# Optimization experiments

Hardware: AMD Instinct MI355X
Metric: run time of the kernel (lower is better)

Reference implementation:

```python
import jax, jax.numpy as jnp
import numpy as np

MAX_CACHE_LEN = 1024
B, S, D, H = 8, 512, 512, 8
DK = D // H


def setup_inputs() -> dict:
    key = jax.random.key(0)
    ks = jax.random.split(key, 11)
    w = lambda k: jax.random.normal(k, (D, D), jnp.float32) * 0.02
    b = lambda k: jax.random.normal(k, (D,), jnp.float32) * 0.02
    return {
        "x": jax.random.normal(ks[0], (B, S, D), jnp.float32),
        "prev_k": jax.random.normal(ks[1], (B, H, MAX_CACHE_LEN, DK), jnp.float32),
        "prev_v": jax.random.normal(ks[2], (B, H, MAX_CACHE_LEN, DK), jnp.float32),
        "Wq": w(ks[3]), "bq": b(ks[4]),
        "Wk": w(ks[5]), "bk": b(ks[6]),
        "Wv": w(ks[7]), "bv": b(ks[8]),
        "Wo": w(ks[9]), "bo": b(ks[10]),
        "offset": MAX_CACHE_LEN,  # cache already full (steady-state streaming)
    }


def reference(x, prev_k, prev_v, Wq, bq, Wk, bk, Wv, bv, Wo, bo, offset):
    Bx, Sx, Dx = x.shape
    Hx = prev_k.shape[1]
    dk = Dx // Hx
    # projections (torch Linear: y = x @ W.T + b), split into heads -> [B,H,S,dk]
    def proj(W, bias):
        return (x @ W.T + bias).reshape(Bx, Sx, Hx, dk).transpose(0, 2, 1, 3)
    q = proj(Wq, bq)
    k = jnp.concatenate([prev_k, proj(Wk, bk)], axis=2)
    v = jnp.concatenate([prev_v, proj(Wv, bv)], axis=2)
    # sliding-window narrow to last MAX_CACHE_LEN keys (static shapes under jit)
    k_full = k.shape[2]
    start = max(0, k_full - MAX_CACHE_LEN)
    k = k[:, :, start:, :]
    v = v[:, :, start:, :]
    k_len = k.shape[2]
    new_offset = min(offset + Sx, MAX_CACHE_LEN)
    # scores [B,H,S,k_len]
    scores = jnp.einsum("bhqd,bhkd->bhqk", q, k) * (dk ** -0.5)
    q_start = new_offset - Sx
    q_idx = jnp.arange(Sx)[:, None] + q_start
    k_idx = jnp.arange(k_len)[None, :]
    mask = q_idx < k_idx  # future keys masked
    scores = jnp.where(mask[None, None], -jnp.inf, scores)
    attn = jax.nn.softmax(scores, axis=-1)
    out = jnp.einsum("bhqk,bhkd->bhqd", attn, v)
    out = out.transpose(0, 2, 1, 3).reshape(Bx, Sx, Dx)
    out = out @ Wo.T + bo
    return out, k, v, jnp.asarray(new_offset, jnp.int64 if jax.config.x64_enabled else jnp.int32)
```

## Files before the change

### kernel.cpp

```cpp
#include <hip/hip_runtime.h>
#include <math.h>

#define B_  8
#define S_  512
#define D_  512
#define H_  8
#define DK_ 64
#define KL_ 1024

typedef __attribute__((ext_vector_type(8))) short bf16x8;
typedef __attribute__((ext_vector_type(4))) float f32x4;

__device__ __forceinline__ unsigned short f2bf(float f) {
    unsigned u = __float_as_uint(f);
    u += 0x7FFF + ((u >> 16) & 1);
    return (unsigned short)(u >> 16);
}
__device__ __forceinline__ float bf2f(unsigned short h) {
    return __uint_as_float(((unsigned)h) << 16);
}

__device__ __forceinline__ void gld16(const void* g, void* l) {
    __builtin_amdgcn_global_load_lds(
        (const __attribute__((address_space(1))) unsigned int*)g,
        (__attribute__((address_space(3))) unsigned int*)l, 16, 0, 0);
}

__global__ __launch_bounds__(256)
void copy_prev_kernel(const float4* __restrict__ pk, const float4* __restrict__ pv,
                      float4* __restrict__ kout, float4* __restrict__ vout,
                      float* __restrict__ off_out) {
    int i = blockIdx.x * 256 + threadIdx.x;
    int bh = i >> 13;
    int r4 = i & 8191;
    kout[bh * 16384 + r4] = pk[bh * 16384 + 8192 + r4];
    vout[bh * 16384 + r4] = pv[bh * 16384 + 8192 + r4];
    if (i == 0) off_out[0] = 1024.0f;
}

__global__ __launch_bounds__(256)
void convert_kernel(const float* __restrict__ x,  const float* __restrict__ Wq,
                    const float* __restrict__ Wk, const float* __restrict__ Wv,
                    unsigned short* __restrict__ xb, unsigned short* __restrict__ Wqb,
                    unsigned short* __restrict__ Wkb, unsigned short* __restrict__ Wvb) {
    int i = blockIdx.x * 256 + threadIdx.x;
    const float* src; unsigned short* dst; int off;
    if (i < 262144)      { src = x;  dst = xb;  off = i; }
    else if (i < 294912) { src = Wq; dst = Wqb; off = i - 262144; }
    else if (i < 327680) { src = Wk; dst = Wkb; off = i - 294912; }
    else                 { src = Wv; dst = Wvb; off = i - 327680; }
    float4 v0 = ((const float4*)src)[off * 2];
    float4 v1 = ((const float4*)src)[off * 2 + 1];
    unsigned short tmp[8] = {f2bf(v0.x), f2bf(v0.y), f2bf(v0.z), f2bf(v0.w),
                             f2bf(v1.x), f2bf(v1.y), f2bf(v1.z), f2bf(v1.w)};
    *(uint4*)&dst[off * 8] = *(uint4*)tmp;
}

template<int MODE>
__device__ __forceinline__
void mfma_gemm_body(const unsigned short* __restrict__ A,
                    const unsigned short* __restrict__ Wb,
                    const float* __restrict__ Wf,
                    const float* __restrict__ bias,
                    float* __restrict__ C32, unsigned short* __restrict__ C16) {
    __shared__ unsigned short As[128 * 32];
    __shared__ unsigned short Bs[128 * 32];
    const int t = threadIdx.x, l = t & 63, w = t >> 6;
    const int m16 = l & 15, quad = l >> 4;
    const int wm = w >> 1, wn = w & 1;
    const int bn = blockIdx.x, bm = blockIdx.y;
    const int arow = l >> 2, acol = (l & 3) * 8;

    f32x4 acc[4][4] = {};

    const unsigned short* Ag = A + (bm * 128) * 512;

    for (int k0 = 0; k0 < 512; k0 += 32) {
        __syncthreads();
        #pragma unroll
        for (int q = 0; q < 2; ++q) {
            int chunk = w * 2 + q;
            gld16(Ag + (chunk * 16 + arow) * 512 + k0 + acol,
                  &As[chunk * 512 + l * 8]);
        }
        if (MODE == 3) {
            const float* Wg = Wf + (bn * 128) * 512 + k0;
            #pragma unroll
            for (int q = 0; q < 2; ++q) {
                int chunk = w * 2 + q;
                const float* src = Wg + (chunk * 16 + arow) * 512 + acol;
                float4 v0 = *(const float4*)src;
                float4 v1 = *(const float4*)(src + 4);
                unsigned short tmp[8] = {f2bf(v0.x), f2bf(v0.y), f2bf(v0.z), f2bf(v0.w),
                                         f2bf(v1.x), f2bf(v1.y), f2bf(v1.z), f2bf(v1.w)};
                *(uint4*)&Bs[chunk * 512 + l * 8] = *(uint4*)tmp;
            }
        } else {
            const unsigned short* Wg = Wb + (bn * 128) * 512 + k0;
            #pragma unroll
            for (int q = 0; q < 2; ++q) {
                int chunk = w * 2 + q;
                gld16(Wg + (chunk * 16 + arow) * 512 + acol,
                      &Bs[chunk * 512 + l * 8]);
            }
        }
        __syncthreads();

        bf16x8 af[4], bfr[4];
        #pragma unroll
        for (int mm = 0; mm < 4; ++mm)
            af[mm] = *(const bf16x8*)&As[(wm * 64 + mm * 16 + m16) * 32 + quad * 8];
        #pragma unroll
        for (int nn = 0; nn < 4; ++nn)
            bfr[nn] = *(const bf16x8*)&Bs[(wn * 64 + nn * 16 + m16) * 32 + quad * 8];
        #pragma unroll
        for (int mm = 0; mm < 4; ++mm)
            #pragma unroll
            for (int nn = 0; nn < 4; ++nn)
                acc[mm][nn] = __builtin_amdgcn_mfma_f32_16x16x32_bf16(
                    af[mm], bfr[nn], acc[mm][nn], 0, 0, 0);
    }

    #pragma unroll
    for (int mm = 0; mm < 4; ++mm) {
        #pragma unroll
        for (int nn = 0; nn < 4; ++nn) {
            int n = bn * 128 + wn * 64 + nn * 16 + m16;
            float bv_ = bias[n];
            #pragma unroll
            for (int r = 0; r < 4; ++r) {
                int m = bm * 128 + wm * 64 + mm * 16 + quad * 4 + r;
                float val = acc[mm][nn][r] + bv_;
                if (MODE == 3) {
                    C32[m * 512 + n] = val;
                } else {
                    int b = m >> 9, s = m & 511;
                    int h = n >> 6, d = n & 63;
                    if (MODE == 1) C16[((b * H_ + h) * S_ + s) * DK_ + d] = f2bf(val * 0.125f);
                    else           C32[((b * H_ + h) * KL_ + 512 + s) * DK_ + d] = val;
                }
            }
        }
    }
}

__global__ __launch_bounds__(256)
void qkv_mfma_kernel(const unsigned short* __restrict__ xb,
                     const unsigned short* __restrict__ Wqb, const float* __restrict__ bq,
                     const unsigned short* __restrict__ Wkb, const float* __restrict__ bk,
                     const unsigned short* __restrict__ Wvb, const float* __restrict__ bv,
                     unsigned short* __restrict__ Qb, float* __restrict__ kout,
                     float* __restrict__ vout) {
    if (blockIdx.z == 0)      mfma_gemm_body<1>(xb, Wqb, nullptr, bq, nullptr, Qb);
    else if (blockIdx.z == 1) mfma_gemm_body<2>(xb, Wkb, nullptr, bk, kout, nullptr);
    else                      mfma_gemm_body<2>(xb, Wvb, nullptr, bv, vout, nullptr);
}

__global__ __launch_bounds__(256)
void out_mfma_kernel(const unsigned short* __restrict__ Ob, const float* __restrict__ Wo,
                     const float* __restrict__ bo, float* __restrict__ C) {
    mfma_gemm_body<3>(Ob, nullptr, Wo, bo, C, nullptr);
}

__global__ __launch_bounds__(256)
void vt_kernel(const float* __restrict__ vout, unsigned short* __restrict__ Vt) {
    __shared__ float Ls[64][68];
    const int kt = blockIdx.x, bh = blockIdx.y;
    const int t = threadIdx.x;
    const float* Vg = vout + (bh * KL_ + (kt << 6)) * DK_;
    #pragma unroll
    for (int it = 0; it < 4; ++it) {
        int idx = t + (it << 8);
        int row = idx >> 4, c4 = idx & 15;
        *(float4*)&Ls[row][c4 << 2] = *(const float4*)&Vg[row * 64 + (c4 << 2)];
    }
    __syncthreads();
    int d = t >> 2, kp = (t & 3) << 4;
    unsigned short tmp[16];
    #pragma unroll
    for (int j = 0; j < 16; ++j) tmp[j] = f2bf(Ls[kp + j][d]);
    unsigned short* dst = Vt + (bh * DK_ + d) * KL_ + (kt << 6) + kp;
    *(uint4*)dst       = *(uint4*)tmp;
    *(uint4*)(dst + 8) = *(uint4*)(tmp + 8);
}

__global__ __launch_bounds__(256)
void attn_kernel(const unsigned short* __restrict__ Qb, const float* __restrict__ K,
                 const unsigned short* __restrict__ Vt, unsigned short* __restrict__ O) {
    const int qt = blockIdx.x, h = blockIdx.y, b = blockIdx.z;
    const int bh = b * H_ + h;
    const int t  = threadIdx.x;
    const int l  = t & 63, w = t >> 6;
    const int m16 = l & 15, quad = l >> 4;

    __shared__ __attribute__((aligned(16))) unsigned short Ks[64][72];
    __shared__ __attribute__((aligned(16))) unsigned short Vts[64][72];
    __shared__ __attribute__((aligned(16))) unsigned short Ps[4][16][72];

    bf16x8 qf[2];
    {
        const unsigned short* qrow = Qb + ((bh * S_) + (qt << 6) + (w << 4) + m16) * DK_;
        qf[0] = *(const bf16x8*)(qrow + quad * 8);
        qf[1] = *(const bf16x8*)(qrow + 32 + quad * 8);
    }

    f32x4 acc_o[4];
    float m_run[4], l_run[4];
    #pragma unroll
    for (int r = 0; r < 4; ++r) {
        m_run[r] = -INFINITY; l_run[r] = 0.f;
        acc_o[r][0] = acc_o[r][1] = acc_o[r][2] = acc_o[r][3] = 0.f;
    }

    const int ktmax = 8 + qt;
    for (int kt = 0; kt <= ktmax; ++kt) {
        __syncthreads();
        {
            const float* Kg = K + (bh * KL_ + (kt << 6)) * DK_;
            #pragma unroll
            for (int it = 0; it < 4; ++it) {
                int idx = t + (it << 8);
                int row = idx >> 4, c4 = idx & 15;
                float4 v = *(const float4*)&Kg[row * 64 + (c4 << 2)];
                ushort4 p;
                p.x = f2bf(v.x); p.y = f2bf(v.y); p.z = f2bf(v.z); p.w = f2bf(v.w);
                *(ushort4*)&Ks[row][c4 << 2] = p;
            }
            const unsigned short* Vg = Vt + (bh * DK_) * KL_ + (kt << 6);
            #pragma unroll
            for (int it = 0; it < 2; ++it) {
                int idx = t + (it << 8);
                int row = idx >> 3, c8 = idx & 7;
                *(uint4*)&Vts[row][c8 << 3] = *(const uint4*)&Vg[row * KL_ + (c8 << 3)];
            }
        }
        __syncthreads();

        f32x4 sacc[4];
        #pragma unroll
        for (int nn = 0; nn < 4; ++nn) {
            sacc[nn][0] = sacc[nn][1] = sacc[nn][2] = sacc[nn][3] = 0.f;
            bf16x8 kf0 = *(const bf16x8*)&Ks[(nn << 4) + m16][quad * 8];
            bf16x8 kf1 = *(const bf16x8*)&Ks[(nn << 4) + m16][32 + quad * 8];
            sacc[nn] = __builtin_amdgcn_mfma_f32_16x16x32_bf16(qf[0], kf0, sacc[nn], 0, 0, 0);
            sacc[nn] = __builtin_amdgcn_mfma_f32_16x16x32_bf16(qf[1], kf1, sacc[nn], 0, 0, 0);
        }

        if (kt == ktmax) {
            int kbase = (kt << 6) + m16;
            int qg512 = (qt << 6) + (w << 4) + (quad << 2) + 512;
            #pragma unroll
            for (int nn = 0; nn < 4; ++nn)
                #pragma unroll
                for (int r = 0; r < 4; ++r)
                    if (kbase + (nn << 4) > qg512 + r) sacc[nn][r] = -INFINITY;
        }

        float mnew[4], alpha[4];
        #pragma unroll
        for (int r = 0; r < 4; ++r) {
            float mx = fmaxf(fmaxf(sacc[0][r], sacc[1][r]), fmaxf(sacc[2][r], sacc[3][r]));
            mx = fmaxf(mx, __shfl_xor(mx, 1));
            mx = fmaxf(mx, __shfl_xor(mx, 2));
            mx = fmaxf(mx, __shfl_xor(mx, 4));
            mx = fmaxf(mx, __shfl_xor(mx, 8));
            mnew[r]  = fmaxf(m_run[r], mx);
            alpha[r] = __expf(m_run[r] - mnew[r]);
            m_run[r] = mnew[r];
        }
        #pragma unroll
        for (int r = 0; r < 4; ++r) {
            float ps = 0.f;
            #pragma unroll
            for (int nn = 0; nn < 4; ++nn) {
                float p = __expf(sacc[nn][r] - mnew[r]);
                ps += p;
                Ps[w][(quad << 2) + r][(nn << 4) + m16] = f2bf(p);
            }
            ps += __shfl_xor(ps, 1);
            ps += __shfl_xor(ps, 2);
            ps += __shfl_xor(ps, 4);
            ps += __shfl_xor(ps, 8);
            l_run[r] = l_run[r] * alpha[r] + ps;
        }
        #pragma unroll
        for (int nn = 0; nn < 4; ++nn)
            #pragma unroll
            for (int r = 0; r < 4; ++r) acc_o[nn][r] *= alpha[r];

        bf16x8 pf0 = *(const bf16x8*)&Ps[w][m16][quad * 8];
        bf16x8 pf1 = *(const bf16x8*)&Ps[w][m16][32 + quad * 8];
        #pragma unroll
        for (int nn = 0; nn < 4; ++nn) {
            bf16x8 vf0 = *(const bf16x8*)&Vts[(nn << 4) + m16][quad * 8];
            bf16x8 vf1 = *(const bf16x8*)&Vts[(nn << 4) + m16][32 + quad * 8];
            acc_o[nn] = __builtin_amdgcn_mfma_f32_16x16x32_bf16(pf0, vf0, acc_o[nn], 0, 0, 0);
            acc_o[nn] = __builtin_amdgcn_mfma_f32_16x16x32_bf16(pf1, vf1, acc_o[nn], 0, 0, 0);
        }
    }

    unsigned short* Og = O + (b * S_ + (qt << 6) + (w << 4)) * D_ + (h << 6);
    #pragma unroll
    for (int r = 0; r < 4; ++r) {
        float inv = 1.f / l_run[r];
        #pragma unroll
        for (int nn = 0; nn < 4; ++nn)
            Og[((quad << 2) + r) * D_ + (nn << 4) + m16] = f2bf(acc_o[nn][r] * inv);
    }
}

extern "C" void kernel_launch(void* const* d_in, const int* in_sizes, int n_in,
                              void* d_out, int out_size, void* d_ws, size_t ws_size,
                              hipStream_t stream) {
    const float* x  = (const float*)d_in[0];
    const float* pk = (const float*)d_in[1];
    const float* pv = (const float*)d_in[2];
    const float* Wq = (const float*)d_in[3];
    const float* bq = (const float*)d_in[4];
    const float* Wk = (const float*)d_in[5];
    const float* bk = (const float*)d_in[6];
    const float* Wv = (const float*)d_in[7];
    const float* bv = (const float*)d_in[8];
    const float* Wo = (const float*)d_in[9];
    const float* bo = (const float*)d_in[10];

    float* out     = (float*)d_out;
    float* kout    = out + 2097152;
    float* vout    = kout + 4194304;
    float* off_out = vout + 4194304;

    unsigned short* Qb  = (unsigned short*)d_ws;
    unsigned short* Vt  = Qb + 2097152;
    unsigned short* xb  = Vt + 4194304;
    unsigned short* Ob  = xb;
    unsigned short* Wqb = Vt;
    unsigned short* Wkb = Wqb + 262144;
    unsigned short* Wvb = Wkb + 262144;

    convert_kernel<<<1408, 256, 0, stream>>>(x, Wq, Wk, Wv, xb, Wqb, Wkb, Wvb);
    copy_prev_kernel<<<2048, 256, 0, stream>>>((const float4*)pk, (const float4*)pv,
                                               (float4*)kout, (float4*)vout, off_out);
    qkv_mfma_kernel<<<dim3(4, 32, 3), 256, 0, stream>>>(xb, Wqb, bq, Wkb, bk, Wvb, bv,
                                                        Qb, kout, vout);
    vt_kernel<<<dim3(16, 64), 256, 0, stream>>>(vout, Vt);
    attn_kernel<<<dim3(8, 8, 8), 256, 0, stream>>>(Qb, kout, Vt, Ob);
    out_mfma_kernel<<<dim3(4, 32), 256, 0, stream>>>(Ob, Wo, bo, out);
}
```

Before: 190.9 us.

## Fuse prep kernels, halve GEMM N-tile, drop LDS staging in attention

Merges the bf16 convert and KV-cache copy kernels into a single prep launch. It halves the GEMM N-tile to 64 so twice as many blocks run, and converts Wo through a perm-based pack in the output GEMM. The attention kernel now gives each wave its own 16-row query tile with its own causal trip count, and reads K (fp32, packed on the fly) and V^T directly from global memory instead of staging them in shared memory behind barriers. Attention output is written in place over Q in head-major layout, and the output GEMM gathers from that layout. This removes barriers and one launch, but repeats global K/V reads per wave, and the cheaper pack truncates to bf16 instead of rounding.

Measured after the change: 225.9 us. +18.3%, slower.

```diff
diff --git a/kernel.cpp b/kernel.cpp
--- a/kernel.cpp
+++ b/kernel.cpp
@@ -16,8 +16,14 @@
     u += 0x7FFF + ((u >> 16) & 1);
     return (unsigned short)(u >> 16);
 }
-__device__ __forceinline__ float bf2f(unsigned short h) {
-    return __uint_as_float(((unsigned)h) << 16);
+__device__ __forceinline__ unsigned pkbf(float lo, float hi) {
+    return __builtin_amdgcn_perm(__float_as_uint(hi), __float_as_uint(lo), 0x07060302u);
+}
+__device__ __forceinline__ bf16x8 pack8(float4 a, float4 b) {
+    union { bf16x8 v; unsigned u[4]; } r;
+    r.u[0] = pkbf(a.x, a.y); r.u[1] = pkbf(a.z, a.w);
+    r.u[2] = pkbf(b.x, b.y); r.u[3] = pkbf(b.z, b.w);
+    return r.v;
 }
 
 __device__ __forceinline__ void gld16(const void* g, void* l) {
@@ -27,33 +33,33 @@
 }
 
 __global__ __launch_bounds__(256)
-void copy_prev_kernel(const float4* __restrict__ pk, const float4* __restrict__ pv,
-                      float4* __restrict__ kout, float4* __restrict__ vout,
-                      float* __restrict__ off_out) {
-    int i = blockIdx.x * 256 + threadIdx.x;
-    int bh = i >> 13;
-    int r4 = i & 8191;
-    kout[bh * 16384 + r4] = pk[bh * 16384 + 8192 + r4];
-    vout[bh * 16384 + r4] = pv[bh * 16384 + 8192 + r4];
-    if (i == 0) off_out[0] = 1024.0f;
-}
-
-__global__ __launch_bounds__(256)
-void convert_kernel(const float* __restrict__ x,  const float* __restrict__ Wq,
-                    const float* __restrict__ Wk, const float* __restrict__ Wv,
-                    unsigned short* __restrict__ xb, unsigned short* __restrict__ Wqb,
-                    unsigned short* __restrict__ Wkb, unsigned short* __restrict__ Wvb) {
-    int i = blockIdx.x * 256 + threadIdx.x;
-    const float* src; unsigned short* dst; int off;
-    if (i < 262144)      { src = x;  dst = xb;  off = i; }
-    else if (i < 294912) { src = Wq; dst = Wqb; off = i - 262144; }
-    else if (i < 327680) { src = Wk; dst = Wkb; off = i - 294912; }
-    else                 { src = Wv; dst = Wvb; off = i - 327680; }
-    float4 v0 = ((const float4*)src)[off * 2];
-    float4 v1 = ((const float4*)src)[off * 2 + 1];
-    unsigned short tmp[8] = {f2bf(v0.x), f2bf(v0.y), f2bf(v0.z), f2bf(v0.w),
-                             f2bf(v1.x), f2bf(v1.y), f2bf(v1.z), f2bf(v1.w)};
-    *(uint4*)&dst[off * 8] = *(uint4*)tmp;
+void prep_kernel(const float* __restrict__ x,  const float* __restrict__ Wq,
+                 const float* __restrict__ Wk, const float* __restrict__ Wv,
+                 const float4* __restrict__ pk, const float4* __restrict__ pv,
+                 unsigned short* __restrict__ xb,  unsigned short* __restrict__ Wqb,
+                 unsigned short* __restrict__ Wkb, unsigned short* __restrict__ Wvb,
+                 float4* __restrict__ kout4, float4* __restrict__ vout4,
+                 float* __restrict__ off_out) {
+    const int blk = blockIdx.x, t = threadIdx.x;
+    if (blk < 1408) {
+        int i = blk * 256 + t;
+        if (i == 0) off_out[0] = 1024.0f;
+        const float* src; unsigned short* dst; int off;
+        if (i < 262144)      { src = x;  dst = xb;  off = i; }
+        else if (i < 294912) { src = Wq; dst = Wqb; off = i - 262144; }
+        else if (i < 327680) { src = Wk; dst = Wkb; off = i - 294912; }
+        else                 { src = Wv; dst = Wvb; off = i - 327680; }
+        float4 v0 = ((const float4*)src)[off * 2];
+        float4 v1 = ((const float4*)src)[off * 2 + 1];
+        unsigned short tmp[8] = {f2bf(v0.x), f2bf(v0.y), f2bf(v0.z), f2bf(v0.w),
+                                 f2bf(v1.x), f2bf(v1.y), f2bf(v1.z), f2bf(v1.w)};
+        *(uint4*)&dst[off * 8] = *(uint4*)tmp;
+    } else {
+        int i = (blk - 1408) * 256 + t;
+        int bh = i >> 13, r4 = i & 8191;
+        kout4[bh * 16384 + r4] = pk[bh * 16384 + 8192 + r4];
+        vout4[bh * 16384 + r4] = pv[bh * 16384 + 8192 + r4];
+    }
 }
 
 template<int MODE>
@@ -64,59 +70,54 @@
                     const float* __restrict__ bias,
                     float* __restrict__ C32, unsigned short* __restrict__ C16) {
     __shared__ unsigned short As[128 * 32];
-    __shared__ unsigned short Bs[128 * 32];
+    __shared__ unsigned short Bs[64 * 32];
     const int t = threadIdx.x, l = t & 63, w = t >> 6;
     const int m16 = l & 15, quad = l >> 4;
     const int wm = w >> 1, wn = w & 1;
     const int bn = blockIdx.x, bm = blockIdx.y;
-    const int arow = l >> 2, acol = (l & 3) * 8;
-
-    f32x4 acc[4][4] = {};
-
-    const unsigned short* Ag = A + (bm * 128) * 512;
+    const int lr = l >> 2, lc = (l & 3) * 8;
+
+    f32x4 acc[4][2] = {};
 
     for (int k0 = 0; k0 < 512; k0 += 32) {
         __syncthreads();
-        #pragma unroll
-        for (int q = 0; q < 2; ++q) {
-            int chunk = w * 2 + q;
-            gld16(Ag + (chunk * 16 + arow) * 512 + k0 + acol,
-                  &As[chunk * 512 + l * 8]);
-        }
         if (MODE == 3) {
-            const float* Wg = Wf + (bn * 128) * 512 + k0;
+            int h = k0 >> 6, dd0 = k0 & 63;
+            const unsigned short* Ab = A + ((((bm >> 2) * 8 + h) * 512) + (bm & 3) * 128) * 64 + dd0;
             #pragma unroll
             for (int q = 0; q < 2; ++q) {
                 int chunk = w * 2 + q;
-                const float* src = Wg + (chunk * 16 + arow) * 512 + acol;
-                float4 v0 = *(const float4*)src;
-                float4 v1 = *(const float4*)(src + 4);
-                unsigned short tmp[8] = {f2bf(v0.x), f2bf(v0.y), f2bf(v0.z), f2bf(v0.w),
-                                         f2bf(v1.x), f2bf(v1.y), f2bf(v1.z), f2bf(v1.w)};
-                *(uint4*)&Bs[chunk * 512 + l * 8] = *(uint4*)tmp;
+                gld16(Ab + (chunk * 16 + lr) * 64 + lc, &As[chunk * 512 + l * 8]);
             }
         } else {
-            const unsigned short* Wg = Wb + (bn * 128) * 512 + k0;
+            const unsigned short* Ab = A + (bm * 128) * 512 + k0;
             #pragma unroll
             for (int q = 0; q < 2; ++q) {
                 int chunk = w * 2 + q;
-                gld16(Wg + (chunk * 16 + arow) * 512 + acol,
-                      &Bs[chunk * 512 + l * 8]);
-            }
+                gld16(Ab + (chunk * 16 + lr) * 512 + lc, &As[chunk * 512 + l * 8]);
+            }
+        }
+        if (MODE == 3) {
+            const float* Wg = Wf + ((bn * 64 + w * 16 + lr) * 512) + k0 + lc;
+            float4 v0 = *(const float4*)Wg;
+            float4 v1 = *(const float4*)(Wg + 4);
+            *(bf16x8*)&Bs[w * 512 + l * 8] = pack8(v0, v1);
+        } else {
+            gld16(Wb + (bn * 64 + w * 16 + lr) * 512 + k0 + lc, &Bs[w * 512 + l * 8]);
         }
         __syncthreads();
 
-        bf16x8 af[4], bfr[4];
+        bf16x8 af[4], bfr[2];
         #pragma unroll
         for (int mm = 0; mm < 4; ++mm)
             af[mm] = *(const bf16x8*)&As[(wm * 64 + mm * 16 + m16) * 32 + quad * 8];
         #pragma unroll
-        for (int nn = 0; nn < 4; ++nn)
-            bfr[nn] = *(const bf16x8*)&Bs[(wn * 64 + nn * 16 + m16) * 32 + quad * 8];
+        for (int nn = 0; nn < 2; ++nn)
+            bfr[nn] = *(const bf16x8*)&Bs[(wn * 32 + nn * 16 + m16) * 32 + quad * 8];
         #pragma unroll
         for (int mm = 0; mm < 4; ++mm)
             #pragma unroll
-            for (int nn = 0; nn < 4; ++nn)
+            for (int nn = 0; nn < 2; ++nn)
                 acc[mm][nn] = __builtin_amdgcn_mfma_f32_16x16x32_bf16(
                     af[mm], bfr[nn], acc[mm][nn], 0, 0, 0);
     }
@@ -124,8 +125,8 @@
     #pragma unroll
     for (int mm = 0; mm < 4; ++mm) {
         #pragma unroll
-        for (int nn = 0; nn < 4; ++nn) {
-            int n = bn * 128 + wn * 64 + nn * 16 + m16;
+        for (int nn = 0; nn < 2; ++nn) {
+            int n = bn * 64 + wn * 32 + nn * 16 + m16;
             float bv_ = bias[n];
             #pragma unroll
             for (int r = 0; r < 4; ++r) {
@@ -185,75 +186,57 @@
 }
 
 __global__ __launch_bounds__(256)
-void attn_kernel(const unsigned short* __restrict__ Qb, const float* __restrict__ K,
-                 const unsigned short* __restrict__ Vt, unsigned short* __restrict__ O) {
-    const int qt = blockIdx.x, h = blockIdx.y, b = blockIdx.z;
-    const int bh = b * H_ + h;
-    const int t  = threadIdx.x;
-    const int l  = t & 63, w = t >> 6;
+void attn_kernel(unsigned short* qo, const float* __restrict__ K,
+                 const unsigned short* __restrict__ Vt) {
+    const int bh = blockIdx.x, qt4 = blockIdx.y;
+    const int t = threadIdx.x, l = t & 63, w = t >> 6;
     const int m16 = l & 15, quad = l >> 4;
-
-    __shared__ __attribute__((aligned(16))) unsigned short Ks[64][72];
-    __shared__ __attribute__((aligned(16))) unsigned short Vts[64][72];
+    const int q0 = (qt4 * 4 + w) * 16;
+
     __shared__ __attribute__((aligned(16))) unsigned short Ps[4][16][72];
 
     bf16x8 qf[2];
     {
-        const unsigned short* qrow = Qb + ((bh * S_) + (qt << 6) + (w << 4) + m16) * DK_;
+        const unsigned short* qrow = qo + (bh * S_ + q0 + m16) * DK_;
         qf[0] = *(const bf16x8*)(qrow + quad * 8);
         qf[1] = *(const bf16x8*)(qrow + 32 + quad * 8);
     }
 
-    f32x4 acc_o[4];
+    f32x4 acc[4];
     float m_run[4], l_run[4];
     #pragma unroll
     for (int r = 0; r < 4; ++r) {
         m_run[r] = -INFINITY; l_run[r] = 0.f;
-        acc_o[r][0] = acc_o[r][1] = acc_o[r][2] = acc_o[r][3] = 0.f;
-    }
-
-    const int ktmax = 8 + qt;
+        acc[r][0] = acc[r][1] = acc[r][2] = acc[r][3] = 0.f;
+    }
+
+    const int ktmax = (527 + q0) >> 6;
+    const float* Kbh = K + (bh * KL_) * DK_;
+    const unsigned short* Vbh = Vt + (bh * DK_) * KL_;
+
     for (int kt = 0; kt <= ktmax; ++kt) {
-        __syncthreads();
-        {
-            const float* Kg = K + (bh * KL_ + (kt << 6)) * DK_;
-            #pragma unroll
-            for (int it = 0; it < 4; ++it) {
-                int idx = t + (it << 8);
-                int row = idx >> 4, c4 = idx & 15;
-                float4 v = *(const float4*)&Kg[row * 64 + (c4 << 2)];
-                ushort4 p;
-                p.x = f2bf(v.x); p.y = f2bf(v.y); p.z = f2bf(v.z); p.w = f2bf(v.w);
-                *(ushort4*)&Ks[row][c4 << 2] = p;
-            }
-            const unsigned short* Vg = Vt + (bh * DK_) * KL_ + (kt << 6);
-            #pragma unroll
-            for (int it = 0; it < 2; ++it) {
-                int idx = t + (it << 8);
-                int row = idx >> 3, c8 = idx & 7;
-                *(uint4*)&Vts[row][c8 << 3] = *(const uint4*)&Vg[row * KL_ + (c8 << 3)];
-            }
-        }
-        __syncthreads();
-
+        const float* Kt = Kbh + (kt << 6) * DK_;
         f32x4 sacc[4];
         #pragma unroll
         for (int nn = 0; nn < 4; ++nn) {
+            const float* kp = Kt + ((nn << 4) + m16) * DK_ + quad * 8;
+            float4 a0 = *(const float4*)kp;
+            float4 b0 = *(const float4*)(kp + 4);
+            float4 a1 = *(const float4*)(kp + 32);
+            float4 b1 = *(const float4*)(kp + 36);
             sacc[nn][0] = sacc[nn][1] = sacc[nn][2] = sacc[nn][3] = 0.f;
-            bf16x8 kf0 = *(const bf16x8*)&Ks[(nn << 4) + m16][quad * 8];
-            bf16x8 kf1 = *(const bf16x8*)&Ks[(nn << 4) + m16][32 + quad * 8];
-            sacc[nn] = __builtin_amdgcn_mfma_f32_16x16x32_bf16(qf[0], kf0, sacc[nn], 0, 0, 0);
-            sacc[nn] = __builtin_amdgcn_mfma_f32_16x16x32_bf16(qf[1], kf1, sacc[nn], 0, 0, 0);
+            sacc[nn] = __builtin_amdgcn_mfma_f32_16x16x32_bf16(qf[0], pack8(a0, b0), sacc[nn], 0, 0, 0);
+            sacc[nn] = __builtin_amdgcn_mfma_f32_16x16x32_bf16(qf[1], pack8(a1, b1), sacc[nn], 0, 0, 0);
         }
 
         if (kt == ktmax) {
-            int kbase = (kt << 6) + m16;
-            int qg512 = (qt << 6) + (w << 4) + (quad << 2) + 512;
-            #pragma unroll
-            for (int nn = 0; nn < 4; ++nn)
+            #pragma unroll
+            for (int nn = 0; nn < 4; ++nn) {
+                int key = (kt << 6) + (nn << 4) + m16;
                 #pragma unroll
                 for (int r = 0; r < 4; ++r)
-                    if (kbase + (nn << 4) > qg512 + r) sacc[nn][r] = -INFINITY;
+                    if (key > 512 + q0 + (quad << 2) + r) sacc[nn][r] = -INFINITY;
+            }
         }
 
         float mnew[4], alpha[4];
@@ -286,26 +269,27 @@
         #pragma unroll
         for (int nn = 0; nn < 4; ++nn)
             #pragma unroll
-            for (int r = 0; r < 4; ++r) acc_o[nn][r] *= alpha[r];
+            for (int r = 0; r < 4; ++r) acc[nn][r] *= alpha[r];
 
         bf16x8 pf0 = *(const bf16x8*)&Ps[w][m16][quad * 8];
         bf16x8 pf1 = *(const bf16x8*)&Ps[w][m16][32 + quad * 8];
         #pragma unroll
         for (int nn = 0; nn < 4; ++nn) {
-            bf16x8 vf0 = *(const bf16x8*)&Vts[(nn << 4) + m16][quad * 8];
-            bf16x8 vf1 = *(const bf16x8*)&Vts[(nn << 4) + m16][32 + quad * 8];
-            acc_o[nn] = __builtin_amdgcn_mfma_f32_16x16x32_bf16(pf0, vf0, acc_o[nn], 0, 0, 0);
-            acc_o[nn] = __builtin_amdgcn_mfma_f32_16x16x32_bf16(pf1, vf1, acc_o[nn], 0, 0, 0);
-        }
-    }
-
-    unsigned short* Og = O + (b * S_ + (qt << 6) + (w << 4)) * D_ + (h << 6);
+            const unsigned short* vp = Vbh + ((nn << 4) + m16) * KL_ + (kt << 6) + quad * 8;
+            bf16x8 vf0 = *(const bf16x8*)vp;
+            bf16x8 vf1 = *(const bf16x8*)(vp + 32);
+            acc[nn] = __builtin_amdgcn_mfma_f32_16x16x32_bf16(pf0, vf0, acc[nn], 0, 0, 0);
+            acc[nn] = __builtin_amdgcn_mfma_f32_16x16x32_bf16(pf1, vf1, acc[nn], 0, 0, 0);
+        }
+    }
+
+    unsigned short* Og = qo + (bh * S_ + q0) * DK_;
     #pragma unroll
     for (int r = 0; r < 4; ++r) {
         float inv = 1.f / l_run[r];
         #pragma unroll
         for (int nn = 0; nn < 4; ++nn)
-            Og[((quad << 2) + r) * D_ + (nn << 4) + m16] = f2bf(acc_o[nn][r] * inv);
+            Og[((quad << 2) + r) * DK_ + (nn << 4) + m16] = f2bf(acc[nn][r] * inv);
     }
 }
 
@@ -332,17 +316,16 @@
     unsigned short* Qb  = (unsigned short*)d_ws;
     unsigned short* Vt  = Qb + 2097152;
     unsigned short* xb  = Vt + 4194304;
-    unsigned short* Ob  = xb;
     unsigned short* Wqb = Vt;
     unsigned short* Wkb = Wqb + 262144;
     unsigned short* Wvb = Wkb + 262144;
 
-    convert_kernel<<<1408, 256, 0, stream>>>(x, Wq, Wk, Wv, xb, Wqb, Wkb, Wvb);
-    copy_prev_kernel<<<2048, 256, 0, stream>>>((const float4*)pk, (const float4*)pv,
-                                               (float4*)kout, (float4*)vout, off_out);
-    qkv_mfma_kernel<<<dim3(4, 32, 3), 256, 0, stream>>>(xb, Wqb, bq, Wkb, bk, Wvb, bv,
+    prep_kernel<<<3456, 256, 0, stream>>>(x, Wq, Wk, Wv, (const float4*)pk, (const float4*)pv,
+                                          xb, Wqb, Wkb, Wvb,
+                                          (float4*)kout, (float4*)vout, off_out);
+    qkv_mfma_kernel<<<dim3(8, 32, 3), 256, 0, stream>>>(xb, Wqb, bq, Wkb, bk, Wvb, bv,
                                                         Qb, kout, vout);
     vt_kernel<<<dim3(16, 64), 256, 0, stream>>>(vout, Vt);
-    attn_kernel<<<dim3(8, 8, 8), 256, 0, stream>>>(Qb, kout, Vt, Ob);
-    out_mfma_kernel<<<dim3(4, 32), 256, 0, stream>>>(Ob, Wo, bo, out);
-}
+    attn_kernel<<<dim3(64, 8), 256, 0, stream>>>(Qb, kout, Vt);
+    out_mfma_kernel<<<dim3(8, 32), 256, 0, stream>>>(Qb, Wo, bo, out);
+}
```
